# Performance work log

Measured on AMD Instinct MI355X. Metric: run time of the kernel, lower is better.

The kernel has to match this reference:

```python
import jax, jax.numpy as jnp
import numpy as np

B, S, IN_DIM, OUT_DIM = 4, 8192, 1024, 1024


def setup_inputs() -> dict:
    key = jax.random.key(0)
    kx, km, kv, kt = jax.random.split(key, 4)
    x = jax.random.normal(kx, (B, S, IN_DIM), dtype=jnp.float32)
    visual_mask = jax.random.randint(km, (B, S), 0, 2) > 0  # bool [B, S]
    # nn.Linear(in_dim, out_dim, bias=False): weight shape [out_dim, in_dim]
    bound = 1.0 / np.sqrt(IN_DIM)
    W_v = jax.random.uniform(kv, (OUT_DIM, IN_DIM), dtype=jnp.float32, minval=-bound, maxval=bound)
    W_t = jax.random.uniform(kt, (OUT_DIM, IN_DIM), dtype=jnp.float32, minval=-bound, maxval=bound)
    return {"x": x, "visual_mask": visual_mask, "W_v": W_v, "W_t": W_t}


def reference(x, visual_mask, W_v, W_t):
    # out = linear_v(x) * mask + linear_t(x) * ~mask
    y_v = jnp.einsum("bsd,od->bso", x, W_v)  # [B, S, OUT_DIM]
    y_t = jnp.einsum("bsd,od->bso", x, W_t)
    m = visual_mask[:, :, None]  # [B, S, 1]
    return jnp.where(m, y_v, y_t)
```

## Files before the change

### kernel.cpp

```cpp
#include <hip/hip_runtime.h>
#include <hip/hip_bf16.h>
#include <stdint.h>

#define M_TOT  32768
#define K_DIM  1024
#define N_DIM  1024

typedef short bf16x8 __attribute__((ext_vector_type(8)));
typedef float f32x4  __attribute__((ext_vector_type(4)));

#define AS1(p) ((__attribute__((address_space(1))) void*)(p))
#define AS3(p) ((__attribute__((address_space(3))) void*)(p))

__device__ __forceinline__ uint32_t packbf2(float a, float b) {
    __hip_bfloat162 h = __float22bfloat162_rn(make_float2(a, b));
    union { __hip_bfloat162 h; uint32_t u; } cvt;
    cvt.h = h;
    return cvt.u;
}

__global__ __launch_bounds__(256) void cvt_kernel(
        const float* __restrict__ x,  const float* __restrict__ wv,
        const float* __restrict__ wt, ushort* __restrict__ xb,
        ushort* __restrict__ dv,      ushort* __restrict__ dt) {
    int t = blockIdx.x * 256 + threadIdx.x;
    const float* src; ushort* dst; int off;
    if (t < 4194304)      { src = x;  dst = xb; off = t * 8; }
    else {
        int u = t - 4194304;
        if (u < 131072)   { src = wv; dst = dv; off = u * 8; }
        else              { src = wt; dst = dt; off = (u - 131072) * 8; }
    }
    float4 a = *(const float4*)(src + off);
    float4 b = *(const float4*)(src + off + 4);
    uint4 p;
    p.x = packbf2(a.x, a.y);
    p.y = packbf2(a.z, a.w);
    p.z = packbf2(b.x, b.y);
    p.w = packbf2(b.z, b.w);
    *(uint4*)(dst + off) = p;
}

__global__ __launch_bounds__(1024) void compact_kernel(
        const int* __restrict__ mask, int* __restrict__ V, int* __restrict__ T,
        int* __restrict__ cnt) {
    const int tid  = threadIdx.x;
    const int lane = tid & 63;
    const int wv   = tid >> 6;

    const int4* mp = (const int4*)mask + tid * 8;
    uint32_t bits = 0;
#pragma unroll
    for (int i = 0; i < 8; ++i) {
        int4 v = mp[i];
        bits |= (uint32_t)(v.x != 0) << (i * 4 + 0);
        bits |= (uint32_t)(v.y != 0) << (i * 4 + 1);
        bits |= (uint32_t)(v.z != 0) << (i * 4 + 2);
        bits |= (uint32_t)(v.w != 0) << (i * 4 + 3);
    }
    int vcnt = __popc(bits);

    int incl = vcnt;
#pragma unroll
    for (int d = 1; d < 64; d <<= 1) {
        int y = __shfl_up(incl, d);
        if (lane >= d) incl += y;
    }
    __shared__ int wsum[16], wexcl[16], totv_s;
    if (lane == 63) wsum[wv] = incl;
    __syncthreads();
    if (tid == 0) {
        int s = 0;
#pragma unroll
        for (int i = 0; i < 16; ++i) { wexcl[i] = s; s += wsum[i]; }
        totv_s = s;
    }
    __syncthreads();
    const int vexcl = wexcl[wv] + incl - vcnt;
    int vbase = vexcl;
    int tbase = tid * 32 - vexcl;

#pragma unroll
    for (int j = 0; j < 32; ++j) {
        int e = tid * 32 + j;
        if ((bits >> j) & 1u) V[vbase++] = e;
        else                  T[tbase++] = e;
    }

    const int Nv = totv_s, Nt = M_TOT - totv_s;
    if (tid == 0) { cnt[0] = Nv; cnt[1] = Nt; }

    __syncthreads();
    const int NBv = (Nv + 127) >> 7, NBt = (Nt + 127) >> 7;
    for (int p = Nv + tid; p < NBv * 128; p += 1024) V[p] = -1;
    for (int p = Nt + tid; p < NBt * 128; p += 1024) T[p] = -1;
}

__global__ __launch_bounds__(256) void gemm_kernel(
        const ushort* __restrict__ xb,
        const ushort* __restrict__ Wv,
        const ushort* __restrict__ Wt,
        const int*    __restrict__ V,
        const int*    __restrict__ T,
        const int*    __restrict__ cnt,
        float*        __restrict__ out) {
    __shared__ ushort sA[128 * 64];
    __shared__ ushort sB[128 * 64];

    const int tid  = threadIdx.x;
    const int lane = tid & 63;
    const int w    = tid >> 6;

    const int kx = blockIdx.x & 7;
    const int bn = (blockIdx.x >> 3) & 7;
    const int gk = blockIdx.x >> 6;
    const int bm = gk * 8 + kx;

    const int Nv  = cnt[0];
    const int Nt  = cnt[1];
    const int NBv = (Nv + 127) >> 7;
    const int NBt = (Nt + 127) >> 7;
    if (bm >= NBv + NBt) return;

    const bool vis = (bm < NBv);
    const int*    rowbase = vis ? (V + (size_t)bm * 128)
                                : (T + (size_t)(bm - NBv) * 128);
    const ushort* W       = vis ? Wv : Wt;
    const int n0 = bn * 128;

    const int trow = tid >> 3;
    const int kcb  = (tid & 7) ^ (trow & 7);
    const ushort* ap[4];
    const ushort* wp[4];
#pragma unroll
    for (int r = 0; r < 4; ++r) {
        int rr = rowbase[r * 32 + trow];
        if (rr < 0) rr = 0;
        ap[r] = xb + (size_t)rr * K_DIM + kcb * 8;
        wp[r] = W + (size_t)(n0 + r * 32 + trow) * K_DIM + kcb * 8;
    }

    const int ml   = lane & 15;
    const int quad = lane >> 4;
    const int wm = (w & 1) * 64;
    const int wn = (w >> 1) * 64;
    uint32_t aoff[2][4], boff[2][4];
#pragma unroll
    for (int ks = 0; ks < 2; ++ks) {
        int kxr = (ks * 4 + quad) ^ (ml & 7);
#pragma unroll
        for (int t = 0; t < 4; ++t) {
            aoff[ks][t] = (uint32_t)(((wm + t * 16 + ml) * 8 + kxr) * 16);
            boff[ks][t] = (uint32_t)(((wn + t * 16 + ml) * 8 + kxr) * 16);
        }
    }

    f32x4 acc[4][4];
#pragma unroll
    for (int i = 0; i < 4; ++i)
#pragma unroll
        for (int j = 0; j < 4; ++j) {
            f32x4 z = {0.f, 0.f, 0.f, 0.f};
            acc[i][j] = z;
        }

    char* sAb = (char*)sA;
    char* sBb = (char*)sB;

    for (int kt = 0; kt < 16; ++kt) {
        const int k0 = kt * 64;
#pragma unroll
        for (int r = 0; r < 4; ++r) {
            char* lb = sBb + (size_t)(r * 256 + w * 64) * 16;
            __builtin_amdgcn_global_load_lds(AS1(wp[r] + k0), AS3(lb), 16, 0, 0);
        }
#pragma unroll
        for (int r = 0; r < 4; ++r) {
            char* la = sAb + (size_t)(r * 256 + w * 64) * 16;
            __builtin_amdgcn_global_load_lds(AS1(ap[r] + k0), AS3(la), 16, 0, 0);
        }
        __syncthreads();
#pragma unroll
        for (int ks = 0; ks < 2; ++ks) {
            bf16x8 af[4], bf[4];
#pragma unroll
            for (int t = 0; t < 4; ++t) af[t] = *(const bf16x8*)(sAb + aoff[ks][t]);
#pragma unroll
            for (int t = 0; t < 4; ++t) bf[t] = *(const bf16x8*)(sBb + boff[ks][t]);
#pragma unroll
            for (int tm = 0; tm < 4; ++tm)
#pragma unroll
                for (int tn = 0; tn < 4; ++tn)
                    acc[tm][tn] = __builtin_amdgcn_mfma_f32_16x16x32_bf16(
                        af[tm], bf[tn], acc[tm][tn], 0, 0, 0);
        }
        __syncthreads();
    }

#pragma unroll
    for (int tm = 0; tm < 4; ++tm) {
        const int rb = wm + tm * 16 + quad * 4;
        int sr0 = rowbase[rb + 0];
        int sr1 = rowbase[rb + 1];
        int sr2 = rowbase[rb + 2];
        int sr3 = rowbase[rb + 3];
#pragma unroll
        for (int tn = 0; tn < 4; ++tn) {
            const int col = n0 + wn + tn * 16 + ml;
            if (sr0 >= 0) out[(size_t)sr0 * N_DIM + col] = acc[tm][tn][0];
            if (sr1 >= 0) out[(size_t)sr1 * N_DIM + col] = acc[tm][tn][1];
            if (sr2 >= 0) out[(size_t)sr2 * N_DIM + col] = acc[tm][tn][2];
            if (sr3 >= 0) out[(size_t)sr3 * N_DIM + col] = acc[tm][tn][3];
        }
    }
}

extern "C" void kernel_launch(void* const* d_in, const int* in_sizes, int n_in,
                              void* d_out, int out_size, void* d_ws, size_t ws_size,
                              hipStream_t stream) {
    const float* x    = (const float*)d_in[0];
    const int*   mask = (const int*)d_in[1];
    const float* Wv   = (const float*)d_in[2];
    const float* Wt   = (const float*)d_in[3];
    float* out = (float*)d_out;

    char* ws = (char*)d_ws;
    ushort* xb  = (ushort*)(ws);
    ushort* dWv = (ushort*)(ws + 67108864);
    ushort* dWt = (ushort*)(ws + 69206016);
    int* V   = (int*)(ws + 71303168);
    int* T   = V + 32768;
    int* cnt = T + 32768;

    cvt_kernel<<<17408, 256, 0, stream>>>(x, Wv, Wt, xb, dWv, dWt);
    compact_kernel<<<1, 1024, 0, stream>>>(mask, V, T, cnt);
    gemm_kernel<<<33 * 64, 256, 0, stream>>>(xb, dWv, dWt, V, T, cnt, out);
}
```

Baseline: 352.5 us.

## Fuse x bf16 conversion into GEMM A-load with double-buffered LDS

Removes the separate pass that converts all of x to bf16. The GEMM now loads fp32 rows of x into registers, converts them and writes them into a double-buffered LDS tile while the current tile is being multiplied. Weight conversion and mask compaction are merged into a single prep kernel, so there is one fewer launch. In exchange, each x row is read as fp32, twice the bytes, and is re-read by all 8 N-blocks. The extra registers and doubled LDS may lower occupancy.

```diff
diff --git a/kernel.cpp b/kernel.cpp
--- a/kernel.cpp
+++ b/kernel.cpp
@@ -19,34 +19,31 @@
     return cvt.u;
 }
 
-__global__ __launch_bounds__(256) void cvt_kernel(
-        const float* __restrict__ x,  const float* __restrict__ wv,
-        const float* __restrict__ wt, ushort* __restrict__ xb,
-        ushort* __restrict__ dv,      ushort* __restrict__ dt) {
-    int t = blockIdx.x * 256 + threadIdx.x;
-    const float* src; ushort* dst; int off;
-    if (t < 4194304)      { src = x;  dst = xb; off = t * 8; }
-    else {
-        int u = t - 4194304;
-        if (u < 131072)   { src = wv; dst = dv; off = u * 8; }
-        else              { src = wt; dst = dt; off = (u - 131072) * 8; }
-    }
-    float4 a = *(const float4*)(src + off);
-    float4 b = *(const float4*)(src + off + 4);
-    uint4 p;
-    p.x = packbf2(a.x, a.y);
-    p.y = packbf2(a.z, a.w);
-    p.z = packbf2(b.x, b.y);
-    p.w = packbf2(b.z, b.w);
-    *(uint4*)(dst + off) = p;
-}
-
-__global__ __launch_bounds__(1024) void compact_kernel(
-        const int* __restrict__ mask, int* __restrict__ V, int* __restrict__ T,
-        int* __restrict__ cnt) {
+__global__ __launch_bounds__(1024) void prep_kernel(
+        const int* __restrict__ mask,
+        const float* __restrict__ wv, const float* __restrict__ wt,
+        ushort* __restrict__ dv, ushort* __restrict__ dt,
+        int* __restrict__ V, int* __restrict__ T, int* __restrict__ cnt) {
+    if (blockIdx.x != 0) {
+        int b = blockIdx.x - 1;
+        int u = b * 8192 + threadIdx.x * 8;
+        const float* src; ushort* dst; int off;
+        if (u < 1048576) { src = wv; dst = dv; off = u; }
+        else             { src = wt; dst = dt; off = u - 1048576; }
+        float4 a0 = *(const float4*)(src + off);
+        float4 a1 = *(const float4*)(src + off + 4);
+        uint4 p;
+        p.x = packbf2(a0.x, a0.y);
+        p.y = packbf2(a0.z, a0.w);
+        p.z = packbf2(a1.x, a1.y);
+        p.w = packbf2(a1.z, a1.w);
+        *(uint4*)(dst + off) = p;
+        return;
+    }
+
     const int tid  = threadIdx.x;
     const int lane = tid & 63;
-    const int wv   = tid >> 6;
+    const int wv_  = tid >> 6;
 
     const int4* mp = (const int4*)mask + tid * 8;
     uint32_t bits = 0;
@@ -67,7 +64,7 @@
         if (lane >= d) incl += y;
     }
     __shared__ int wsum[16], wexcl[16], totv_s;
-    if (lane == 63) wsum[wv] = incl;
+    if (lane == 63) wsum[wv_] = incl;
     __syncthreads();
     if (tid == 0) {
         int s = 0;
@@ -76,7 +73,7 @@
         totv_s = s;
     }
     __syncthreads();
-    const int vexcl = wexcl[wv] + incl - vcnt;
+    const int vexcl = wexcl[wv_] + incl - vcnt;
     int vbase = vexcl;
     int tbase = tid * 32 - vexcl;
 
@@ -97,15 +94,15 @@
 }
 
 __global__ __launch_bounds__(256) void gemm_kernel(
-        const ushort* __restrict__ xb,
+        const float*  __restrict__ x,
         const ushort* __restrict__ Wv,
         const ushort* __restrict__ Wt,
         const int*    __restrict__ V,
         const int*    __restrict__ T,
         const int*    __restrict__ cnt,
         float*        __restrict__ out) {
-    __shared__ ushort sA[128 * 64];
-    __shared__ ushort sB[128 * 64];
+    __shared__ ushort sA[2][128 * 64];
+    __shared__ ushort sB[2][128 * 64];
 
     const int tid  = threadIdx.x;
     const int lane = tid & 63;
@@ -130,14 +127,14 @@
 
     const int trow = tid >> 3;
     const int kcb  = (tid & 7) ^ (trow & 7);
-    const ushort* ap[4];
+    const float*  apf[4];
     const ushort* wp[4];
 #pragma unroll
     for (int r = 0; r < 4; ++r) {
         int rr = rowbase[r * 32 + trow];
         if (rr < 0) rr = 0;
-        ap[r] = xb + (size_t)rr * K_DIM + kcb * 8;
-        wp[r] = W + (size_t)(n0 + r * 32 + trow) * K_DIM + kcb * 8;
+        apf[r] = x + (size_t)rr * K_DIM + kcb * 8;
+        wp[r]  = W + (size_t)(n0 + r * 32 + trow) * K_DIM + kcb * 8;
     }
 
     const int ml   = lane & 15;
@@ -164,35 +161,75 @@
             acc[i][j] = z;
         }
 
-    char* sAb = (char*)sA;
-    char* sBb = (char*)sB;
-
+    char* sAb[2] = { (char*)sA[0], (char*)sA[1] };
+    char* sBb[2] = { (char*)sB[0], (char*)sB[1] };
+
+#pragma unroll
+    for (int r = 0; r < 4; ++r) {
+        char* lb = sBb[0] + (size_t)(r * 256 + w * 64) * 16;
+        __builtin_amdgcn_global_load_lds(AS1(wp[r]), AS3(lb), 16, 0, 0);
+    }
+    float4 a[8];
+#pragma unroll
+    for (int r = 0; r < 4; ++r) {
+        a[r * 2]     = *(const float4*)(apf[r]);
+        a[r * 2 + 1] = *(const float4*)(apf[r] + 4);
+    }
+#pragma unroll
+    for (int r = 0; r < 4; ++r) {
+        uint4 p;
+        p.x = packbf2(a[r * 2].x,     a[r * 2].y);
+        p.y = packbf2(a[r * 2].z,     a[r * 2].w);
+        p.z = packbf2(a[r * 2 + 1].x, a[r * 2 + 1].y);
+        p.w = packbf2(a[r * 2 + 1].z, a[r * 2 + 1].w);
+        *(uint4*)(sAb[0] + (size_t)(r * 256 + tid) * 16) = p;
+    }
+    __syncthreads();
+
+#pragma unroll
     for (int kt = 0; kt < 16; ++kt) {
-        const int k0 = kt * 64;
-#pragma unroll
-        for (int r = 0; r < 4; ++r) {
-            char* lb = sBb + (size_t)(r * 256 + w * 64) * 16;
-            __builtin_amdgcn_global_load_lds(AS1(wp[r] + k0), AS3(lb), 16, 0, 0);
-        }
-#pragma unroll
-        for (int r = 0; r < 4; ++r) {
-            char* la = sAb + (size_t)(r * 256 + w * 64) * 16;
-            __builtin_amdgcn_global_load_lds(AS1(ap[r] + k0), AS3(la), 16, 0, 0);
-        }
-        __syncthreads();
+        const int k0  = kt * 64;
+        const int cur = kt & 1;
+        const int nxt = cur ^ 1;
+
+        if (kt < 15) {
+#pragma unroll
+            for (int r = 0; r < 4; ++r) {
+                char* lb = sBb[nxt] + (size_t)(r * 256 + w * 64) * 16;
+                __builtin_amdgcn_global_load_lds(AS1(wp[r] + k0 + 64), AS3(lb), 16, 0, 0);
+            }
+#pragma unroll
+            for (int r = 0; r < 4; ++r) {
+                a[r * 2]     = *(const float4*)(apf[r] + k0 + 64);
+                a[r * 2 + 1] = *(const float4*)(apf[r] + k0 + 68);
+            }
+        }
+
 #pragma unroll
         for (int ks = 0; ks < 2; ++ks) {
-            bf16x8 af[4], bf[4];
-#pragma unroll
-            for (int t = 0; t < 4; ++t) af[t] = *(const bf16x8*)(sAb + aoff[ks][t]);
-#pragma unroll
-            for (int t = 0; t < 4; ++t) bf[t] = *(const bf16x8*)(sBb + boff[ks][t]);
+            bf16x8 af[4], bfr[4];
+#pragma unroll
+            for (int t = 0; t < 4; ++t) af[t]  = *(const bf16x8*)(sAb[cur] + aoff[ks][t]);
+#pragma unroll
+            for (int t = 0; t < 4; ++t) bfr[t] = *(const bf16x8*)(sBb[cur] + boff[ks][t]);
 #pragma unroll
             for (int tm = 0; tm < 4; ++tm)
 #pragma unroll
                 for (int tn = 0; tn < 4; ++tn)
                     acc[tm][tn] = __builtin_amdgcn_mfma_f32_16x16x32_bf16(
-                        af[tm], bf[tn], acc[tm][tn], 0, 0, 0);
+                        af[tm], bfr[tn], acc[tm][tn], 0, 0, 0);
+        }
+
+        if (kt < 15) {
+#pragma unroll
+            for (int r = 0; r < 4; ++r) {
+                uint4 p;
+                p.x = packbf2(a[r * 2].x,     a[r * 2].y);
+                p.y = packbf2(a[r * 2].z,     a[r * 2].w);
+                p.z = packbf2(a[r * 2 + 1].x, a[r * 2 + 1].y);
+                p.w = packbf2(a[r * 2 + 1].z, a[r * 2 + 1].w);
+                *(uint4*)(sAb[nxt] + (size_t)(r * 256 + tid) * 16) = p;
+            }
         }
         __syncthreads();
     }
@@ -225,14 +262,12 @@
     float* out = (float*)d_out;
 
     char* ws = (char*)d_ws;
-    ushort* xb  = (ushort*)(ws);
-    ushort* dWv = (ushort*)(ws + 67108864);
-    ushort* dWt = (ushort*)(ws + 69206016);
-    int* V   = (int*)(ws + 71303168);
+    ushort* dWv = (ushort*)(ws);
+    ushort* dWt = (ushort*)(ws + (1 << 21));
+    int* V   = (int*)(ws + (1 << 22));
     int* T   = V + 32768;
     int* cnt = T + 32768;
 
-    cvt_kernel<<<17408, 256, 0, stream>>>(x, Wv, Wt, xb, dWv, dWt);
-    compact_kernel<<<1, 1024, 0, stream>>>(mask, V, T, cnt);
-    gemm_kernel<<<33 * 64, 256, 0, stream>>>(xb, dWv, dWt, V, T, cnt, out);
-}
+    prep_kernel<<<257, 1024, 0, stream>>>(mask, Wv, Wt, dWv, dWt, V, T, cnt);
+    gemm_kernel<<<33 * 64, 256, 0, stream>>>(x, dWv, dWt, V, T, cnt, out);
+}
```

After: 398.7 us. +13.1%, slower.
